# Kernel tuning notes

Measured on AMD Instinct MI355X. Metric: run time of the kernel, lower is better.

## Reference

```python
import jax, jax.numpy as jnp
import numpy as np

B, LU, LV, D = 16, 2048, 2048, 1024


def setup_inputs() -> dict:
    key = jax.random.key(0)
    ku, kv, kl, kw = jax.random.split(key, 4)
    u = jax.random.normal(ku, (B, LU, D), dtype=jnp.float32)
    v = jax.random.normal(kv, (B, LV, D), dtype=jnp.float32)
    # padding mask: True = masked position; every batch keeps >= LV//2 valid tokens
    lengths = jax.random.randint(kl, (B,), LV // 2, LV + 1)
    v_mask = jnp.arange(LV)[None, :] >= lengths[:, None]  # [B, LV] bool
    # Linear(input_size=D, output_size=D) parameters
    W = jax.random.normal(kw, (D, D), dtype=jnp.float32) * (1.0 / np.sqrt(D))
    b = jnp.zeros((D,), dtype=jnp.float32)
    return {"u": u, "v": v, "v_mask": v_mask, "W": W, "b": b}


def reference(u, v, v_mask, W, b):
    # shared ReLU-projected bilinear attention
    u_ = jax.nn.relu(u @ W.T + b)            # [B, Lu, D]
    v_ = jax.nn.relu(v @ W.T + b)            # [B, Lv, D]
    alpha = jnp.einsum("bud,bvd->buv", u_, v_)  # [B, Lu, Lv]
    alpha = jnp.where(v_mask[:, None, :], -jnp.inf, alpha)
    alpha = jax.nn.softmax(alpha, axis=-1)
    return jnp.einsum("buv,bvd->bud", alpha, v)  # [B, Lu, D]
```

## Files before the change

kernel.cpp:

```cpp
#include <hip/hip_runtime.h>
#include <math.h>

#define B_  16
#define LU_ 2048
#define LV_ 2048
#define D_  1024
#define NT_ (LV_ / 128)
#define MB_ (1024ull * 1024ull)

typedef __attribute__((ext_vector_type(8))) short ush8;
typedef __attribute__((ext_vector_type(8))) _Float16 f16x8;
typedef __attribute__((ext_vector_type(4))) float f32x4;

__device__ __forceinline__ unsigned short f2h(float x) {
    _Float16 h = (_Float16)x;
    return __builtin_bit_cast(unsigned short, h);
}

__device__ __forceinline__ void gload_lds16(const void* g, void* l) {
    __builtin_amdgcn_global_load_lds(
        (const __attribute__((address_space(1))) void*)g,
        (__attribute__((address_space(3))) void*)l, 16, 0, 0);
}

__global__ void lengths_kernel(const void* __restrict__ mask, int* __restrict__ lengths) {
    __shared__ int viol;
    __shared__ int cnt[B_];
    const int t = threadIdx.x;
    if (t == 0) viol = 0;
    if (t < B_) cnt[t] = 0;
    __syncthreads();
    const unsigned char* mb = (const unsigned char*)mask;
    int local = 0;
    for (int i = t; i < B_ * LV_ - 1; i += 256) {
        if (((i + 1) % LV_) != 0) {
            if (mb[i] != 0 && mb[i + 1] == 0) local++;
        }
    }
    if (local) atomicAdd(&viol, local);
    __syncthreads();
    const bool is_i32 = (viol > 0);
    const int b = t >> 4, s = t & 15;
    int c = 0;
    if (is_i32) {
        const int* mi = (const int*)mask;
        for (int v2 = s; v2 < LV_; v2 += 16) c += (mi[b * LV_ + v2] == 0) ? 1 : 0;
    } else {
        for (int v2 = s; v2 < LV_; v2 += 16) c += (mb[b * LV_ + v2] == 0) ? 1 : 0;
    }
    atomicAdd(&cnt[b], c);
    __syncthreads();
    if (t < B_) lengths[t] = cnt[t];
}

__global__ __launch_bounds__(256) void cvt_kernel(
    const float* __restrict__ X, unsigned short* __restrict__ Y, long n8) {
    const long stride = (long)gridDim.x * 256;
    for (long i = (long)blockIdx.x * 256 + threadIdx.x; i < n8; i += stride) {
        float4 x0 = ((const float4*)X)[i * 2];
        float4 x1 = ((const float4*)X)[i * 2 + 1];
        float xv[8] = {x0.x, x0.y, x0.z, x0.w, x1.x, x1.y, x1.z, x1.w};
        ush8 h;
#pragma unroll
        for (int j = 0; j < 8; j++) h[j] = (short)f2h(xv[j]);
        ((ush8*)Y)[i] = h;
    }
}

__global__ __launch_bounds__(256, 2) void proj_kernel(
    const unsigned short* __restrict__ Xf, const unsigned short* __restrict__ Wf,
    const float* __restrict__ bias, const int* __restrict__ lengths, int is_v,
    unsigned short* __restrict__ Yf) {
    if (is_v) {
        const int bb = blockIdx.x >> 4;
        const int lv0 = (blockIdx.x & 15) * 128;
        if (lv0 >= lengths[bb]) return;
    }
    __shared__ alignas(16) unsigned short sA[128 * 64], sB[128 * 64];
    const int t = threadIdx.x, lane = t & 63, w = t >> 6;
    const int fr = lane & 15, fg = lane >> 4;
    const int row0 = blockIdx.x * 128, col0 = blockIdx.y * 128;

    size_t aog[4], bog[4];
    int dbs[4];
#pragma unroll
    for (int i = 0; i < 4; i++) {
        const int r = w * 32 + i * 8 + (lane >> 3);
        const int cg = (lane & 7) ^ (r & 7);
        aog[i] = (size_t)(row0 + r) * D_ + cg * 8;
        bog[i] = (size_t)(col0 + r) * D_ + cg * 8;
        dbs[i] = (w * 32 + i * 8) * 64;
    }
    int aoff[2][2], boff[2][8];
#pragma unroll
    for (int kk = 0; kk < 2; kk++) {
#pragma unroll
        for (int m = 0; m < 2; m++) {
            const int r = w * 32 + m * 16 + fr;
            aoff[kk][m] = r * 64 + (((kk * 4 + fg) ^ (r & 7))) * 8;
        }
#pragma unroll
        for (int n = 0; n < 8; n++) {
            const int r = n * 16 + fr;
            boff[kk][n] = r * 64 + (((kk * 4 + fg) ^ (r & 7))) * 8;
        }
    }

    const f32x4 fzero = {0.f, 0.f, 0.f, 0.f};
    f32x4 acc[2][8];
#pragma unroll
    for (int m = 0; m < 2; m++)
#pragma unroll
        for (int n = 0; n < 8; n++) acc[m][n] = fzero;

#pragma unroll 1
    for (int k0 = 0; k0 < D_; k0 += 64) {
        __syncthreads();
#pragma unroll
        for (int i = 0; i < 4; i++) {
            gload_lds16(Xf + aog[i] + k0, &sA[dbs[i]]);
            gload_lds16(Wf + bog[i] + k0, &sB[dbs[i]]);
        }
        __syncthreads();
#pragma unroll
        for (int kk = 0; kk < 2; kk++) {
            const f16x8 a0 = *(const f16x8*)&sA[aoff[kk][0]];
            const f16x8 a1 = *(const f16x8*)&sA[aoff[kk][1]];
#pragma unroll
            for (int n = 0; n < 8; n++) {
                const f16x8 bv = *(const f16x8*)&sB[boff[kk][n]];
                acc[0][n] = __builtin_amdgcn_mfma_f32_16x16x32_f16(a0, bv, acc[0][n], 0, 0, 0);
                acc[1][n] = __builtin_amdgcn_mfma_f32_16x16x32_f16(a1, bv, acc[1][n], 0, 0, 0);
            }
        }
    }

#pragma unroll
    for (int m = 0; m < 2; m++)
#pragma unroll
        for (int n = 0; n < 8; n++) {
            const int col = col0 + n * 16 + fr;
            const float bv = bias[col];
#pragma unroll
            for (int j = 0; j < 4; j++) {
                const int row = row0 + w * 32 + m * 16 + fg * 4 + j;
                const float y = fmaxf(acc[m][n][j] + bv, 0.f);
                Yf[(size_t)row * D_ + col] = f2h(y);
            }
        }
}

__global__ __launch_bounds__(256) void transpose_v_kernel(
    const float* __restrict__ V, unsigned short* __restrict__ VT,
    unsigned short* __restrict__ Vraw) {
    __shared__ unsigned short s[64 * 72];
    const int b = blockIdx.z;
    const int v0 = blockIdx.x * 64, d0 = blockIdx.y * 64;
    const int t = threadIdx.x;
    {
        const int r = t >> 2, q = (t & 3) * 16;
        const float* src = V + ((size_t)b * LV_ + v0 + r) * D_ + d0 + q;
        unsigned short hb[16];
#pragma unroll
        for (int i = 0; i < 4; i++) {
            float4 x = ((const float4*)src)[i];
            hb[i * 4 + 0] = f2h(x.x);
            hb[i * 4 + 1] = f2h(x.y);
            hb[i * 4 + 2] = f2h(x.z);
            hb[i * 4 + 3] = f2h(x.w);
        }
#pragma unroll
        for (int j = 0; j < 16; j++) s[r * 72 + q + j] = hb[j];
        unsigned short* rdst = Vraw + ((size_t)b * LV_ + v0 + r) * D_ + d0 + q;
        ((ush8*)rdst)[0] = *(ush8*)&hb[0];
        ((ush8*)rdst)[1] = *(ush8*)&hb[8];
    }
    __syncthreads();
    {
        const int d = t >> 2, vq = (t & 3) * 16;
        ush8 t0, t1;
#pragma unroll
        for (int j = 0; j < 8; j++) t0[j] = (short)s[(vq + j) * 72 + d];
#pragma unroll
        for (int j = 0; j < 8; j++) t1[j] = (short)s[(vq + 8 + j) * 72 + d];
        unsigned short* dst = VT + ((size_t)b * D_ + d0 + d) * LV_ + v0 + vq;
        ((ush8*)dst)[0] = t0;
        ((ush8*)dst)[1] = t1;
    }
}

__global__ __launch_bounds__(256, 2) void attn_logits_kernel(
    const unsigned short* __restrict__ Uf, const unsigned short* __restrict__ Vf,
    const int* __restrict__ lengths,
    unsigned short* __restrict__ Pp, float* __restrict__ m_used,
    float* __restrict__ Z_used) {
    __shared__ alignas(16) unsigned short sU[128 * 64], sV[128 * 64];
    const int b = blockIdx.z, ut = blockIdx.x, vt = blockIdx.y;
    const int t = threadIdx.x, lane = t & 63, w = t >> 6;
    const int fr = lane & 15, fg = lane >> 4;
    const int length = lengths[b];
    const int row0 = ut * 128, col0 = vt * 128;

    if (col0 >= length) {
        if (t < 128) {
            const size_t row = (size_t)b * LU_ + row0 + t;
            m_used[row * NT_ + vt] = -__builtin_inff();
            Z_used[row * NT_ + vt] = 0.f;
        }
        return;
    }

    size_t aog[4], bog[4];
    int dbs[4];
#pragma unroll
    for (int i = 0; i < 4; i++) {
        const int r = w * 32 + i * 8 + (lane >> 3);
        const int cg = (lane & 7) ^ (r & 7);
        aog[i] = ((size_t)b * LU_ + row0 + r) * D_ + cg * 8;
        bog[i] = ((size_t)b * LV_ + col0 + r) * D_ + cg * 8;
        dbs[i] = (w * 32 + i * 8) * 64;
    }
    int aoff[2][2], boff[2][8];
#pragma unroll
    for (int kk = 0; kk < 2; kk++) {
#pragma unroll
        for (int m = 0; m < 2; m++) {
            const int r = w * 32 + m * 16 + fr;
            aoff[kk][m] = r * 64 + (((kk * 4 + fg) ^ (r & 7))) * 8;
        }
#pragma unroll
        for (int n = 0; n < 8; n++) {
            const int r = n * 16 + fr;
            boff[kk][n] = r * 64 + (((kk * 4 + fg) ^ (r & 7))) * 8;
        }
    }

    const f32x4 fzero = {0.f, 0.f, 0.f, 0.f};
    f32x4 acc[2][8];
#pragma unroll
    for (int m = 0; m < 2; m++)
#pragma unroll
        for (int n = 0; n < 8; n++) acc[m][n] = fzero;

#pragma unroll 1
    for (int k0 = 0; k0 < D_; k0 += 64) {
        __syncthreads();
#pragma unroll
        for (int i = 0; i < 4; i++) {
            gload_lds16(Uf + aog[i] + k0, &sU[dbs[i]]);
            gload_lds16(Vf + bog[i] + k0, &sV[dbs[i]]);
        }
        __syncthreads();
#pragma unroll
        for (int kk = 0; kk < 2; kk++) {
            const f16x8 a0 = *(const f16x8*)&sU[aoff[kk][0]];
            const f16x8 a1 = *(const f16x8*)&sU[aoff[kk][1]];
#pragma unroll
            for (int n = 0; n < 8; n++) {
                const f16x8 bv = *(const f16x8*)&sV[boff[kk][n]];
                acc[0][n] = __builtin_amdgcn_mfma_f32_16x16x32_f16(a0, bv, acc[0][n], 0, 0, 0);
                acc[1][n] = __builtin_amdgcn_mfma_f32_16x16x32_f16(a1, bv, acc[1][n], 0, 0, 0);
            }
        }
    }

#pragma unroll
    for (int m = 0; m < 2; m++) {
        float mt[4] = {-__builtin_inff(), -__builtin_inff(), -__builtin_inff(), -__builtin_inff()};
#pragma unroll
        for (int n = 0; n < 8; n++) {
            const int col = col0 + n * 16 + fr;
            if (col < length) {
#pragma unroll
                for (int j = 0; j < 4; j++) mt[j] = fmaxf(mt[j], acc[m][n][j]);
            }
        }
#pragma unroll
        for (int d = 1; d < 16; d <<= 1) {
#pragma unroll
            for (int j = 0; j < 4; j++) mt[j] = fmaxf(mt[j], __shfl_xor(mt[j], d));
        }
        float rs[4] = {0.f, 0.f, 0.f, 0.f};
#pragma unroll
        for (int n = 0; n < 8; n++) {
            const int col = col0 + n * 16 + fr;
            const bool valid = (col < length);
#pragma unroll
            for (int j = 0; j < 4; j++) {
                const float p = valid ? __expf(acc[m][n][j] - mt[j]) : 0.f;
                rs[j] += p;
                const size_t row = (size_t)b * LU_ + row0 + w * 32 + m * 16 + fg * 4 + j;
                Pp[row * LV_ + col] = f2h(p);
            }
        }
#pragma unroll
        for (int d = 1; d < 16; d <<= 1) {
#pragma unroll
            for (int j = 0; j < 4; j++) rs[j] += __shfl_xor(rs[j], d);
        }
        if (fr == 0) {
#pragma unroll
            for (int j = 0; j < 4; j++) {
                const size_t row = (size_t)b * LU_ + row0 + w * 32 + m * 16 + fg * 4 + j;
                m_used[row * NT_ + vt] = mt[j];
                Z_used[row * NT_ + vt] = rs[j];
            }
        }
    }
}

__global__ __launch_bounds__(256) void stats_combine_kernel(
    const float* __restrict__ m_used, const float* __restrict__ Z_used,
    float* __restrict__ Sc) {
    const int row = blockIdx.x * 256 + threadIdx.x;
    float mv[NT_];
    float m = -__builtin_inff();
#pragma unroll
    for (int i = 0; i < NT_; i++) {
        mv[i] = m_used[(size_t)row * NT_ + i];
        m = fmaxf(m, mv[i]);
    }
    float ev[NT_];
    float z = 0.f;
#pragma unroll
    for (int i = 0; i < NT_; i++) {
        ev[i] = __expf(mv[i] - m);
        z += Z_used[(size_t)row * NT_ + i] * ev[i];
    }
    const float inv = 1.f / z;
#pragma unroll
    for (int i = 0; i < NT_; i++) Sc[(size_t)row * NT_ + i] = ev[i] * inv;
}

__global__ __launch_bounds__(256, 4) void pv_gemm_kernel(
    const unsigned short* __restrict__ Pp, const unsigned short* __restrict__ VT,
    const float* __restrict__ Sc, const int* __restrict__ lengths,
    float* __restrict__ Out) {
    __shared__ alignas(16) unsigned short sA[128 * 64], sB[128 * 64];
    __shared__ float sSc[NT_ * 128];
    const int b = blockIdx.z, bm = blockIdx.x, bn = blockIdx.y;
    const int t = threadIdx.x, lane = t & 63, w = t >> 6;
    const int wr = (w >> 1) * 64, wc = (w & 1) * 64;
    const int fr = lane & 15, fg = lane >> 4;
    const int length = lengths[b];
    const int ntv = (length + 127) >> 7;

    if (t < 128) {
        const float* scrow = Sc + ((size_t)b * LU_ + bm * 128 + t) * NT_;
        float4 s0 = ((const float4*)scrow)[0];
        float4 s1 = ((const float4*)scrow)[1];
        float4 s2 = ((const float4*)scrow)[2];
        float4 s3 = ((const float4*)scrow)[3];
        float sv[16] = {s0.x, s0.y, s0.z, s0.w, s1.x, s1.y, s1.z, s1.w,
                        s2.x, s2.y, s2.z, s2.w, s3.x, s3.y, s3.z, s3.w};
#pragma unroll
        for (int j = 0; j < NT_; j++) sSc[j * 128 + t] = sv[j];
    }
    __syncthreads();

    size_t aog[4], bog[4];
    int dbs[4];
#pragma unroll
    for (int i = 0; i < 4; i++) {
        const int r = w * 32 + i * 8 + (lane >> 3);
        const int cg = (lane & 7) ^ (r & 7);
        aog[i] = ((size_t)b * LU_ + bm * 128 + r) * LV_ + cg * 8;
        bog[i] = ((size_t)b * D_ + bn * 128 + r) * LV_ + cg * 8;
        dbs[i] = (w * 32 + i * 8) * 64;
    }
    int aoff[2][4], boff[2][4];
#pragma unroll
    for (int kk = 0; kk < 2; kk++) {
#pragma unroll
        for (int m = 0; m < 4; m++) {
            const int r = wr + m * 16 + fr;
            aoff[kk][m] = r * 64 + (((kk * 4 + fg) ^ (r & 7))) * 8;
        }
#pragma unroll
        for (int n = 0; n < 4; n++) {
            const int r = wc + n * 16 + fr;
            boff[kk][n] = r * 64 + (((kk * 4 + fg) ^ (r & 7))) * 8;
        }
    }

    const f32x4 fzero = {0.f, 0.f, 0.f, 0.f};
    f32x4 acc[4][4];
#pragma unroll
    for (int m = 0; m < 4; m++)
#pragma unroll
        for (int n = 0; n < 4; n++) acc[m][n] = fzero;

#pragma unroll 1
    for (int vt = 0; vt < ntv; ++vt) {
        f16x8 scv[4];
#pragma unroll
        for (int m = 0; m < 4; m++) {
            const _Float16 sh = (_Float16)sSc[vt * 128 + wr + m * 16 + fr];
#pragma unroll
            for (int j = 0; j < 8; j++) scv[m][j] = sh;
        }

#pragma unroll 1
        for (int kb = 0; kb < 2; ++kb) {
            const int k0 = vt * 128 + kb * 64;
            __syncthreads();
#pragma unroll
            for (int i = 0; i < 4; i++) {
                gload_lds16(Pp + aog[i] + k0, &sA[dbs[i]]);
                gload_lds16(VT + bog[i] + k0, &sB[dbs[i]]);
            }
            __syncthreads();
#pragma unroll
            for (int kk = 0; kk < 2; kk++) {
                f16x8 af[4];
#pragma unroll
                for (int m = 0; m < 4; m++)
                    af[m] = (*(const f16x8*)&sA[aoff[kk][m]]) * scv[m];
#pragma unroll
                for (int n = 0; n < 4; n++) {
                    const f16x8 bv = *(const f16x8*)&sB[boff[kk][n]];
#pragma unroll
                    for (int m = 0; m < 4; m++)
                        acc[m][n] = __builtin_amdgcn_mfma_f32_16x16x32_f16(af[m], bv, acc[m][n], 0, 0, 0);
                }
            }
        }
    }

    float* Ob = Out + (size_t)b * LU_ * D_;
#pragma unroll
    for (int m = 0; m < 4; m++) {
        const int rbase = bm * 128 + wr + m * 16 + fg * 4;
#pragma unroll
        for (int n = 0; n < 4; n++) {
            const int col = bn * 128 + wc + n * 16 + fr;
#pragma unroll
            for (int j = 0; j < 4; j++)
                Ob[(size_t)(rbase + j) * D_ + col] = acc[m][n][j];
        }
    }
}

extern "C" void kernel_launch(void* const* d_in, const int* in_sizes, int n_in,
                              void* d_out, int out_size, void* d_ws, size_t ws_size,
                              hipStream_t stream) {
    (void)in_sizes; (void)n_in; (void)out_size; (void)ws_size;
    const float* u    = (const float*)d_in[0];
    const float* v    = (const float*)d_in[1];
    const void*  vm   = d_in[2];
    const float* W    = (const float*)d_in[3];
    const float* bias = (const float*)d_in[4];
    float* out = (float*)d_out;
    char* ws = (char*)d_ws;

    unsigned short* Pp    = (unsigned short*)(ws + 0 * MB_);
    unsigned short* vT    = (unsigned short*)(ws + 128 * MB_);
    unsigned short* u_f   = (unsigned short*)(ws + 192 * MB_);
    unsigned short* v_f   = (unsigned short*)(ws + 256 * MB_);
    unsigned short* vraw  = (unsigned short*)(ws + 320 * MB_);
    unsigned short* xs_u  = (unsigned short*)(ws + 384 * MB_);
    unsigned short* W_f   = (unsigned short*)(ws + 448 * MB_);
    int*   lengths = (int*)(ws + 450 * MB_);
    float* m_used  = (float*)(ws + 451 * MB_);
    float* Z_used  = (float*)(ws + 453 * MB_);
    float* Sc      = (float*)(ws + 455 * MB_);

    const long nW8 = (long)D_ * D_ / 8;
    const long nX8 = (long)B_ * LU_ * D_ / 8;

    lengths_kernel<<<1, 256, 0, stream>>>(vm, lengths);
    cvt_kernel<<<512, 256, 0, stream>>>(W, W_f, nW8);
    cvt_kernel<<<4096, 256, 0, stream>>>(u, xs_u, nX8);
    proj_kernel<<<dim3(B_ * LU_ / 128, D_ / 128), 256, 0, stream>>>(
        xs_u, W_f, bias, lengths, 0, u_f);
    transpose_v_kernel<<<dim3(LV_ / 64, D_ / 64, B_), 256, 0, stream>>>(v, vT, vraw);
    proj_kernel<<<dim3(B_ * LV_ / 128, D_ / 128), 256, 0, stream>>>(
        vraw, W_f, bias, lengths, 1, v_f);
    attn_logits_kernel<<<dim3(LU_ / 128, NT_, B_), 256, 0, stream>>>(
        u_f, v_f, lengths, Pp, m_used, Z_used);
    stats_combine_kernel<<<B_ * LU_ / 256, 256, 0, stream>>>(m_used, Z_used, Sc);
    pv_gemm_kernel<<<dim3(LU_ / 128, D_ / 128, B_), 256, 0, stream>>>(Pp, vT, Sc, lengths, out);
}
```

Measured before the change: 584.8 us.

## Fuse softmax stats combine into PV GEMM and skip masked V transpose tiles

Removes the separate stats_combine kernel. Each PV GEMM block now recomputes the per-tile max and normalizer scales for its 128 rows directly from m_used and Z_used, which saves a launch and the Sc round trip through memory. The V transpose/convert kernel also exits early for 64-row tiles beyond the 128-rounded valid length, skipping conversion work for padded tokens. The cost is redundant stats recomputation across the 8 column blocks. The early exit also leaves vraw and vT uninitialized past the valid length, so downstream kernels must never read those rows.

```diff
diff --git a/kernel.cpp b/kernel.cpp
--- a/kernel.cpp
+++ b/kernel.cpp
@@ -151,11 +151,12 @@
 }
 
 __global__ __launch_bounds__(256) void transpose_v_kernel(
-    const float* __restrict__ V, unsigned short* __restrict__ VT,
-    unsigned short* __restrict__ Vraw) {
+    const float* __restrict__ V, const int* __restrict__ lengths,
+    unsigned short* __restrict__ VT, unsigned short* __restrict__ Vraw) {
     __shared__ unsigned short s[64 * 72];
     const int b = blockIdx.z;
     const int v0 = blockIdx.x * 64, d0 = blockIdx.y * 64;
+    if (v0 >= ((lengths[b] + 127) & ~127)) return;
     const int t = threadIdx.x;
     {
         const int r = t >> 2, q = (t & 3) * 16;
@@ -309,33 +310,10 @@
     }
 }
 
-__global__ __launch_bounds__(256) void stats_combine_kernel(
-    const float* __restrict__ m_used, const float* __restrict__ Z_used,
-    float* __restrict__ Sc) {
-    const int row = blockIdx.x * 256 + threadIdx.x;
-    float mv[NT_];
-    float m = -__builtin_inff();
-#pragma unroll
-    for (int i = 0; i < NT_; i++) {
-        mv[i] = m_used[(size_t)row * NT_ + i];
-        m = fmaxf(m, mv[i]);
-    }
-    float ev[NT_];
-    float z = 0.f;
-#pragma unroll
-    for (int i = 0; i < NT_; i++) {
-        ev[i] = __expf(mv[i] - m);
-        z += Z_used[(size_t)row * NT_ + i] * ev[i];
-    }
-    const float inv = 1.f / z;
-#pragma unroll
-    for (int i = 0; i < NT_; i++) Sc[(size_t)row * NT_ + i] = ev[i] * inv;
-}
-
 __global__ __launch_bounds__(256, 4) void pv_gemm_kernel(
     const unsigned short* __restrict__ Pp, const unsigned short* __restrict__ VT,
-    const float* __restrict__ Sc, const int* __restrict__ lengths,
-    float* __restrict__ Out) {
+    const float* __restrict__ m_used, const float* __restrict__ Z_used,
+    const int* __restrict__ lengths, float* __restrict__ Out) {
     __shared__ alignas(16) unsigned short sA[128 * 64], sB[128 * 64];
     __shared__ float sSc[NT_ * 128];
     const int b = blockIdx.z, bm = blockIdx.x, bn = blockIdx.y;
@@ -346,15 +324,24 @@
     const int ntv = (length + 127) >> 7;
 
     if (t < 128) {
-        const float* scrow = Sc + ((size_t)b * LU_ + bm * 128 + t) * NT_;
-        float4 s0 = ((const float4*)scrow)[0];
-        float4 s1 = ((const float4*)scrow)[1];
-        float4 s2 = ((const float4*)scrow)[2];
-        float4 s3 = ((const float4*)scrow)[3];
-        float sv[16] = {s0.x, s0.y, s0.z, s0.w, s1.x, s1.y, s1.z, s1.w,
-                        s2.x, s2.y, s2.z, s2.w, s3.x, s3.y, s3.z, s3.w};
-#pragma unroll
-        for (int j = 0; j < NT_; j++) sSc[j * 128 + t] = sv[j];
+        const size_t row = (size_t)b * LU_ + bm * 128 + t;
+        float mv[NT_];
+        float m = -__builtin_inff();
+#pragma unroll
+        for (int i = 0; i < NT_; i++) {
+            mv[i] = m_used[row * NT_ + i];
+            m = fmaxf(m, mv[i]);
+        }
+        float ev[NT_];
+        float z = 0.f;
+#pragma unroll
+        for (int i = 0; i < NT_; i++) {
+            ev[i] = __expf(mv[i] - m);
+            z += Z_used[row * NT_ + i] * ev[i];
+        }
+        const float inv = 1.f / z;
+#pragma unroll
+        for (int i = 0; i < NT_; i++) sSc[i * 128 + t] = ev[i] * inv;
     }
     __syncthreads();
 
@@ -463,7 +450,6 @@
     int*   lengths = (int*)(ws + 450 * MB_);
     float* m_used  = (float*)(ws + 451 * MB_);
     float* Z_used  = (float*)(ws + 453 * MB_);
-    float* Sc      = (float*)(ws + 455 * MB_);
 
     const long nW8 = (long)D_ * D_ / 8;
     const long nX8 = (long)B_ * LU_ * D_ / 8;
@@ -473,11 +459,11 @@
     cvt_kernel<<<4096, 256, 0, stream>>>(u, xs_u, nX8);
     proj_kernel<<<dim3(B_ * LU_ / 128, D_ / 128), 256, 0, stream>>>(
         xs_u, W_f, bias, lengths, 0, u_f);
-    transpose_v_kernel<<<dim3(LV_ / 64, D_ / 64, B_), 256, 0, stream>>>(v, vT, vraw);
+    transpose_v_kernel<<<dim3(LV_ / 64, D_ / 64, B_), 256, 0, stream>>>(v, lengths, vT, vraw);
     proj_kernel<<<dim3(B_ * LV_ / 128, D_ / 128), 256, 0, stream>>>(
         vraw, W_f, bias, lengths, 1, v_f);
     attn_logits_kernel<<<dim3(LU_ / 128, NT_, B_), 256, 0, stream>>>(
         u_f, v_f, lengths, Pp, m_used, Z_used);
-    stats_combine_kernel<<<B_ * LU_ / 256, 256, 0, stream>>>(m_used, Z_used, Sc);
-    pv_gemm_kernel<<<dim3(LU_ / 128, D_ / 128, B_), 256, 0, stream>>>(Pp, vT, Sc, lengths, out);
-}
+    pv_gemm_kernel<<<dim3(LU_ / 128, D_ / 128, B_), 256, 0, stream>>>(
+        Pp, vT, m_used, Z_used, lengths, out);
+}
```

New measurement: 575.3 us, median of 2. Within noise of the previous version (-1.6%).
